# Optimization experiments

Measured on AMD Instinct MI355X. Metric: run time of the kernel, lower is better.

The kernel has to match this reference:

```python
import jax, jax.numpy as jnp
import numpy as np

B, L, D, H = 32, 1024, 1024, 1024

def setup_inputs() -> dict:
    key = jax.random.key(0)
    k1, k2, k3 = jax.random.split(key, 3)
    query = jax.random.normal(k1, (B, L, D), dtype=jnp.float32)
    keys = jax.random.normal(k2, (B, L, D), dtype=jnp.float32)
    # xavier_normal for Linear(D, H): std = sqrt(2/(D+H))
    W = jax.random.normal(k3, (H, D), dtype=jnp.float32) * np.sqrt(2.0 / (D + H)).astype(np.float32)
    b = jnp.zeros((H,), dtype=jnp.float32)
    return {"query": query, "keys": keys, "W": W, "b": b}

def reference(query, keys, W, b):
    # L2-normalize along feature dim (matches torch .norm(dim=-1, keepdim=True))
    qn = query / jnp.linalg.norm(query, axis=-1, keepdims=True)
    kn = keys / jnp.linalg.norm(keys, axis=-1, keepdims=True)
    # scores[b,i,j] = <kn[b,i], qn[b,j]>  ->  [B, Lk, Lq]
    scores = jnp.einsum('bid,bjd->bij', kn, qn)
    attn = jax.nn.softmax(scores, axis=-1)
    # bmm(attn, keys) then sum over batch -> [L, D]
    out = jnp.einsum('bij,bjd->id', attn, keys)
    x = jax.nn.relu(out @ W.T + b)
    return (x, attn)
```

## Files before the change

kernel.cpp:

```cpp
#include <hip/hip_runtime.h>
#include <hip/hip_bf16.h>

#define NBATCH 32
#define Ls 1024
#define Ds 1024
#define Hs 1024

typedef float f32x4 __attribute__((ext_vector_type(4)));
typedef __bf16 v8bf __attribute__((ext_vector_type(8)));
typedef unsigned short u16x8 __attribute__((ext_vector_type(8)));
typedef unsigned short u16x4 __attribute__((ext_vector_type(4)));
typedef __hip_bfloat16 bf16;

__device__ __forceinline__ float bfbits2f(unsigned short h) {
  unsigned u = ((unsigned)h) << 16;
  return __builtin_bit_cast(float, u);
}
__device__ __forceinline__ unsigned short f2b(float x) {
  return __builtin_bit_cast(unsigned short, __float2bfloat16(x));
}
__device__ __forceinline__ u16x8 pack8(const float4& a, const float4& b, float s) {
  u16x8 r;
  r[0] = f2b(a.x * s); r[1] = f2b(a.y * s); r[2] = f2b(a.z * s); r[3] = f2b(a.w * s);
  r[4] = f2b(b.x * s); r[5] = f2b(b.y * s); r[6] = f2b(b.z * s); r[7] = f2b(b.w * s);
  return r;
}

__global__ __launch_bounds__(256) void k_convq(const float* __restrict__ q,
                                               bf16* __restrict__ qn) {
  const int w0 = ((int)blockIdx.x * 256 + (int)threadIdx.x) >> 6;
  const int lane = threadIdx.x & 63;
  #pragma unroll
  for (int it = 0; it < 2; ++it) {
    const size_t r0 = ((size_t)(it * 8192 + w0)) * 2;
    const float4* q0 = reinterpret_cast<const float4*>(q + r0 * Ds);
    float4 qv[2][4];
    #pragma unroll
    for (int rr = 0; rr < 2; ++rr)
      #pragma unroll
      for (int h = 0; h < 2; ++h) {
        qv[rr][h * 2 + 0] = q0[rr * 256 + h * 128 + lane * 2 + 0];
        qv[rr][h * 2 + 1] = q0[rr * 256 + h * 128 + lane * 2 + 1];
      }
    float sq0 = 0.f, sq1 = 0.f;
    #pragma unroll
    for (int p = 0; p < 4; ++p) {
      sq0 += qv[0][p].x*qv[0][p].x + qv[0][p].y*qv[0][p].y + qv[0][p].z*qv[0][p].z + qv[0][p].w*qv[0][p].w;
      sq1 += qv[1][p].x*qv[1][p].x + qv[1][p].y*qv[1][p].y + qv[1][p].z*qv[1][p].z + qv[1][p].w*qv[1][p].w;
    }
    #pragma unroll
    for (int o = 1; o < 64; o <<= 1) { sq0 += __shfl_xor(sq0, o); sq1 += __shfl_xor(sq1, o); }
    const float iq0 = 1.0f / sqrtf(sq0), iq1 = 1.0f / sqrtf(sq1);
    u16x8* qo = reinterpret_cast<u16x8*>(qn + r0 * Ds);
    qo[lane]        = pack8(qv[0][0], qv[0][1], iq0);
    qo[64 + lane]   = pack8(qv[0][2], qv[0][3], iq0);
    qo[128 + lane]  = pack8(qv[1][0], qv[1][1], iq1);
    qo[192 + lane]  = pack8(qv[1][2], qv[1][3], iq1);
  }
}

__global__ __launch_bounds__(256) void k_convkT(const float* __restrict__ k,
                                                bf16* __restrict__ kb,
                                                bf16* __restrict__ kT,
                                                float* __restrict__ invk) {
  __shared__ float tile[64][65];
  __shared__ float red[4][16][16];
  const int b = blockIdx.y;
  const int j0 = blockIdx.x * 64;
  const int t = threadIdx.x;
  const int jr = t >> 4;
  const int cg = t & 15;
  const int c4 = cg * 4;
  const float* src = k + (size_t)b * Ls * Ds + (size_t)j0 * Ds;
  bf16* kbd = kb + (size_t)b * Ls * Ds + (size_t)j0 * Ds;
  bf16* kTd = kT + (size_t)b * Ds * Ls + j0;
  float ssq[4] = {0.f, 0.f, 0.f, 0.f};

  for (int dc = 0; dc < 16; ++dc) {
    const int d0 = dc * 64;
    float4 v[4];
    #pragma unroll
    for (int rr = 0; rr < 4; ++rr) {
      const int j = jr + rr * 16;
      v[rr] = *reinterpret_cast<const float4*>(&src[(size_t)j * Ds + d0 + c4]);
      ssq[rr] += v[rr].x*v[rr].x + v[rr].y*v[rr].y + v[rr].z*v[rr].z + v[rr].w*v[rr].w;
      u16x4 o = { f2b(v[rr].x), f2b(v[rr].y), f2b(v[rr].z), f2b(v[rr].w) };
      *reinterpret_cast<u16x4*>(&kbd[(size_t)j * Ds + d0 + c4]) = o;
    }
    __syncthreads();
    #pragma unroll
    for (int rr = 0; rr < 4; ++rr) {
      const int j = jr + rr * 16;
      tile[j][c4 + 0] = v[rr].x; tile[j][c4 + 1] = v[rr].y;
      tile[j][c4 + 2] = v[rr].z; tile[j][c4 + 3] = v[rr].w;
    }
    __syncthreads();
    #pragma unroll
    for (int rr = 0; rr < 4; ++rr) {
      const int dd = jr + rr * 16;
      u16x4 o = { f2b(tile[c4 + 0][dd]), f2b(tile[c4 + 1][dd]),
                  f2b(tile[c4 + 2][dd]), f2b(tile[c4 + 3][dd]) };
      *reinterpret_cast<u16x4*>(&kTd[(size_t)(d0 + dd) * Ls + c4]) = o;
    }
  }

  #pragma unroll
  for (int rr = 0; rr < 4; ++rr) red[rr][jr][cg] = ssq[rr];
  __syncthreads();
  if (t < 64) {
    const int r = (t & 15) + (t >> 4) * 16;
    float s = 0.f;
    #pragma unroll
    for (int c = 0; c < 16; ++c) s += red[t >> 4][t & 15][c];
    invk[(size_t)b * Ls + j0 + r] = 1.0f / sqrtf(s);
  }
}

__global__ __launch_bounds__(256) void k_w2(const float* __restrict__ W,
                                            bf16* __restrict__ W2) {
  const size_t idx = (size_t)blockIdx.x * 256 + threadIdx.x;
  const size_t e0 = idx * 4;
  const size_t h = e0 >> 10, d = e0 & 1023;
  const float4 w = reinterpret_cast<const float4*>(W)[idx];
  u16x4 wh = { f2b(w.x), f2b(w.y), f2b(w.z), f2b(w.w) };
  u16x4 wl = { f2b(w.x - bfbits2f(wh[0])), f2b(w.y - bfbits2f(wh[1])),
               f2b(w.z - bfbits2f(wh[2])), f2b(w.w - bfbits2f(wh[3])) };
  bf16* row = W2 + h * 3072;
  *reinterpret_cast<u16x4*>(row + d) = wh;
  *reinterpret_cast<u16x4*>(row + 1024 + d) = wh;
  *reinterpret_cast<u16x4*>(row + 2048 + d) = wl;
}

template<int KT, int MODE>
__global__ __launch_bounds__(512) void k_gemm256(
    const bf16* __restrict__ A, const bf16* __restrict__ B,
    void* __restrict__ Cv, const float* __restrict__ scale,
    int lda, int ldb, int ldc, int nb,
    size_t sA, size_t sB, size_t zA, size_t zB, size_t zC, size_t zS)
{
  __shared__ bf16 lds[2][2][256 * 64];
  const int tid = threadIdx.x;
  const int lane = tid & 63;
  const int wid = tid >> 6;
  const int wr = wid >> 2;
  const int wc = wid & 3;
  const int bid = blockIdx.x;
  const int bz = (bid & 7) + 8 * (bid >> 7);
  const int wq = (bid >> 3) & 15;
  const size_t n0 = (size_t)(wq & 3) * 256;
  const size_t m0 = (size_t)(wq >> 2) * 256;
  const bf16* Az = A + (size_t)bz * zA;
  const bf16* Bz = B + (size_t)bz * zB;

  const int srow = tid >> 3;
  const int sslot = tid & 7;
  f32x4 acc[8][4] = {};

  auto stageChunk = [&](int tt, int ab, int c, int buf) {
    const int bb = tt / KT;
    const int k0 = (tt - bb * KT) * 64;
    const int row = c * 64 + srow;
    const int ksl = (sslot ^ (row & 7)) * 8;
    const bf16* src = (ab == 0)
        ? (Az + (size_t)bb * sA + (m0 + row) * lda + k0 + ksl)
        : (Bz + (size_t)bb * sB + (n0 + row) * ldb + k0 + ksl);
    __builtin_amdgcn_global_load_lds(
        (const __attribute__((address_space(1))) void*)src,
        (__attribute__((address_space(3))) void*)(&lds[buf][ab][c * 4096 + tid * 8]), 16, 0, 0);
  };

  const int rsel = lane & 15, qd = lane >> 4;
  v8bf a0[4][2], a1[4][2], b[4][2];

  auto readAinto = [&](v8bf (&dst)[4][2], const bf16* As, int mh) {
    #pragma unroll
    for (int m = 0; m < 4; ++m) {
      const int r = wr * 128 + mh * 64 + m * 16 + rsel;
      #pragma unroll
      for (int h = 0; h < 2; ++h) {
        const int s = (h * 4 + qd) ^ (r & 7);
        dst[m][h] = *reinterpret_cast<const v8bf*>(reinterpret_cast<const char*>(As) + r * 128 + s * 16);
      }
    }
  };
  auto readB2 = [&](const bf16* Bs, int npair) {
    #pragma unroll
    for (int n = 0; n < 2; ++n) {
      const int r = wc * 64 + (npair * 2 + n) * 16 + rsel;
      #pragma unroll
      for (int h = 0; h < 2; ++h) {
        const int s = (h * 4 + qd) ^ (r & 7);
        b[npair * 2 + n][h] = *reinterpret_cast<const v8bf*>(reinterpret_cast<const char*>(Bs) + r * 128 + s * 16);
      }
    }
  };
  auto mfmaQ = [&](v8bf (&aa)[4][2], int mh, int npair) {
    __builtin_amdgcn_s_setprio(1);
    #pragma unroll
    for (int m = 0; m < 4; ++m)
      #pragma unroll
      for (int n = 0; n < 2; ++n) {
        const int mi = mh * 4 + m, ni = npair * 2 + n;
        acc[mi][ni] = __builtin_amdgcn_mfma_f32_16x16x32_bf16(aa[m][0], b[ni][0], acc[mi][ni], 0, 0, 0);
        acc[mi][ni] = __builtin_amdgcn_mfma_f32_16x16x32_bf16(aa[m][1], b[ni][1], acc[mi][ni], 0, 0, 0);
      }
    __builtin_amdgcn_s_setprio(0);
  };

  const int T = KT * nb;

  #pragma unroll
  for (int c = 0; c < 4; ++c) stageChunk(0, 0, c, 0);
  #pragma unroll
  for (int c = 0; c < 4; ++c) stageChunk(0, 1, c, 0);
  #pragma unroll
  for (int c = 0; c < 4; ++c) stageChunk(1, 0, c, 1);
  #pragma unroll
  for (int c = 0; c < 4; ++c) stageChunk(1, 1, c, 1);
  asm volatile("s_waitcnt vmcnt(8)" ::: "memory");
  __builtin_amdgcn_s_barrier();

  for (int t = 0; t < T; ++t) {
    const int d = t & 1;
    const bf16* As = lds[d][0];
    const bf16* Bs = lds[d][1];
    const int u = t + 2;
    const bool st = (u < T);

    readAinto(a0, As, 0);
    readB2(Bs, 0);
    __builtin_amdgcn_sched_barrier(0);
    readB2(Bs, 1);
    __builtin_amdgcn_sched_barrier(0);
    readAinto(a1, As, 1);
    __builtin_amdgcn_sched_barrier(0);

    asm volatile("s_waitcnt lgkmcnt(12)" ::: "memory");
    __builtin_amdgcn_sched_barrier(0);
    mfmaQ(a0, 0, 0);
    asm volatile("s_waitcnt lgkmcnt(8)" ::: "memory");
    __builtin_amdgcn_sched_barrier(0);
    mfmaQ(a0, 0, 1);
    asm volatile("s_waitcnt lgkmcnt(0)" ::: "memory");
    __builtin_amdgcn_sched_barrier(0);
    __builtin_amdgcn_s_barrier();
    if (st) {
      stageChunk(u, 0, 0, d); stageChunk(u, 0, 1, d);
      stageChunk(u, 0, 2, d); stageChunk(u, 0, 3, d);
      stageChunk(u, 1, 0, d); stageChunk(u, 1, 1, d);
      stageChunk(u, 1, 2, d); stageChunk(u, 1, 3, d);
    }
    __builtin_amdgcn_sched_barrier(0);
    mfmaQ(a1, 1, 1);
    mfmaQ(a1, 1, 0);
    if (t < T - 1) {
      if (st) { asm volatile("s_waitcnt vmcnt(8)" ::: "memory"); }
      else    { asm volatile("s_waitcnt vmcnt(0)" ::: "memory"); }
      __builtin_amdgcn_s_barrier();
    }
  }

  if (MODE == 0) {
    float* Cz = (float*)Cv + (size_t)bz * zC;
    #pragma unroll
    for (int m = 0; m < 8; ++m) {
      const size_t ri = m0 + wr * 128 + m * 16 + (size_t)((lane >> 4) * 4);
      #pragma unroll
      for (int n = 0; n < 4; ++n) {
        const size_t cj = n0 + wc * 64 + n * 16 + (lane & 15);
        #pragma unroll
        for (int r = 0; r < 4; ++r)
          Cz[(ri + r) * ldc + cj] = acc[m][n][r];
      }
    }
  } else {
    bf16* Cz = (bf16*)Cv + (size_t)bz * zC;
    const float* Sz = scale + (size_t)bz * zS;
    #pragma unroll
    for (int m = 0; m < 8; ++m) {
      const size_t ri = m0 + wr * 128 + m * 16 + (size_t)((lane >> 4) * 4);
      const float4 ik = *reinterpret_cast<const float4*>(Sz + ri);
      #pragma unroll
      for (int n = 0; n < 4; ++n) {
        const size_t cj = n0 + wc * 64 + n * 16 + (lane & 15);
        Cz[(ri + 0) * ldc + cj] = __float2bfloat16(acc[m][n][0] * ik.x);
        Cz[(ri + 1) * ldc + cj] = __float2bfloat16(acc[m][n][1] * ik.y);
        Cz[(ri + 2) * ldc + cj] = __float2bfloat16(acc[m][n][2] * ik.z);
        Cz[(ri + 3) * ldc + cj] = __float2bfloat16(acc[m][n][3] * ik.w);
      }
    }
  }
}

__global__ __launch_bounds__(256) void k_gemm_nt(
    const bf16* __restrict__ A, const bf16* __restrict__ B,
    float* __restrict__ C,
    int lda, int ldb, int ldc, int K,
    size_t zA, size_t zB, size_t zC)
{
  __shared__ bf16 As[128 * 32];
  __shared__ bf16 Bs[128 * 32];
  const int tid = threadIdx.x;
  const int lane = tid & 63;
  const int wc = (tid >> 6) & 1;
  const int wr = (tid >> 7) & 1;
  const size_t m0 = (size_t)blockIdx.y * 128;
  const size_t n0 = (size_t)blockIdx.x * 128;
  const bf16* Az = A + (size_t)blockIdx.z * zA;
  const bf16* Bz = B + (size_t)blockIdx.z * zB;
  float* Cz = C + (size_t)blockIdx.z * zC;
  f32x4 acc[4][4] = {};

  const int beta0 = tid * 16;
  const int row0 = tid >> 2;
  const int kk0 = ((tid & 3) ^ ((row0 >> 1) & 3)) * 8;
  const int sw = (((lane >> 4) ^ ((lane >> 1) & 3)) << 4);
  const int rsel = lane & 15;

  for (int k0 = 0; k0 < K; k0 += 32) {
    __syncthreads();
    __builtin_amdgcn_global_load_lds(
        (const __attribute__((address_space(1))) void*)(Az + (m0 + row0) * lda + (k0 + kk0)),
        (__attribute__((address_space(3))) void*)(&As[beta0 / 2]), 16, 0, 0);
    __builtin_amdgcn_global_load_lds(
        (const __attribute__((address_space(1))) void*)(Az + (m0 + row0 + 64) * lda + (k0 + kk0)),
        (__attribute__((address_space(3))) void*)(&As[beta0 / 2 + 2048]), 16, 0, 0);
    __builtin_amdgcn_global_load_lds(
        (const __attribute__((address_space(1))) void*)(Bz + (n0 + row0) * ldb + (k0 + kk0)),
        (__attribute__((address_space(3))) void*)(&Bs[beta0 / 2]), 16, 0, 0);
    __builtin_amdgcn_global_load_lds(
        (const __attribute__((address_space(1))) void*)(Bz + (n0 + row0 + 64) * ldb + (k0 + kk0)),
        (__attribute__((address_space(3))) void*)(&Bs[beta0 / 2 + 2048]), 16, 0, 0);
    __syncthreads();

    v8bf af[4], bg[4];
    #pragma unroll
    for (int m = 0; m < 4; ++m) {
      const int rA = wr * 64 + m * 16 + rsel;
      af[m] = *reinterpret_cast<const v8bf*>(reinterpret_cast<const char*>(As) + rA * 64 + sw);
      const int rB = wc * 64 + m * 16 + rsel;
      bg[m] = *reinterpret_cast<const v8bf*>(reinterpret_cast<const char*>(Bs) + rB * 64 + sw);
    }
    #pragma unroll
    for (int m = 0; m < 4; ++m)
      #pragma unroll
      for (int n = 0; n < 4; ++n)
        acc[m][n] = __builtin_amdgcn_mfma_f32_16x16x32_bf16(af[m], bg[n], acc[m][n], 0, 0, 0);
  }

  #pragma unroll
  for (int m = 0; m < 4; ++m) {
    const size_t ri = m0 + wr * 64 + m * 16 + ((lane >> 4) * 4);
    #pragma unroll
    for (int n = 0; n < 4; ++n) {
      const size_t cj = n0 + wc * 64 + n * 16 + (lane & 15);
      #pragma unroll
      for (int r = 0; r < 4; ++r)
        Cz[(ri + r) * ldc + cj] = acc[m][n][r];
    }
  }
}

__global__ __launch_bounds__(256) void k_softmax(const bf16* __restrict__ sc,
                                                 float* __restrict__ attn,
                                                 bf16* __restrict__ abf) {
  const int wave = ((int)blockIdx.x * 256 + (int)threadIdx.x) >> 6;
  const int lane = threadIdx.x & 63;
  for (int i = 0; i < 4; ++i) {
    const size_t row = (size_t)wave * 4 + i;
    const u16x8* sr = reinterpret_cast<const u16x8*>(sc + row * Ls);
    const u16x8 s0 = sr[lane], s1 = sr[lane + 64];
    float e[16];
    float ss = 0.f;
    #pragma unroll
    for (int j = 0; j < 8; ++j) { e[j] = __expf(bfbits2f(s0[j])); ss += e[j]; }
    #pragma unroll
    for (int j = 0; j < 8; ++j) { e[8 + j] = __expf(bfbits2f(s1[j])); ss += e[8 + j]; }
    #pragma unroll
    for (int o = 1; o < 64; o <<= 1) ss += __shfl_xor(ss, o);
    const float inv = 1.0f / ss;
    #pragma unroll
    for (int j = 0; j < 16; ++j) e[j] *= inv;
    float4* ar = reinterpret_cast<float4*>(attn + row * Ls);
    float4 a0 = {e[0], e[1], e[2], e[3]},   a1 = {e[4], e[5], e[6], e[7]};
    float4 a2 = {e[8], e[9], e[10], e[11]}, a3 = {e[12], e[13], e[14], e[15]};
    ar[lane * 2 + 0] = a0;  ar[lane * 2 + 1] = a1;
    ar[128 + lane * 2 + 0] = a2;  ar[128 + lane * 2 + 1] = a3;
    u16x8* ab8 = reinterpret_cast<u16x8*>(abf + row * Ls);
    u16x8 b0, b1;
    #pragma unroll
    for (int j = 0; j < 8; ++j) { b0[j] = f2b(e[j]); b1[j] = f2b(e[8 + j]); }
    ab8[lane] = b0;
    ab8[64 + lane] = b1;
  }
}

__global__ __launch_bounds__(256) void k_reduce(const float* __restrict__ part,
                                                bf16* __restrict__ A2) {
  const size_t idx = (size_t)blockIdx.x * 256 + threadIdx.x;
  float4 s = {0.f, 0.f, 0.f, 0.f};
  #pragma unroll
  for (int g = 0; g < 16; ++g) {
    const float4 p = reinterpret_cast<const float4*>(part + (size_t)g * (Ls * Ds))[idx];
    s.x += p.x; s.y += p.y; s.z += p.z; s.w += p.w;
  }
  const size_t e0 = idx * 4;
  const size_t i = e0 >> 10, d = e0 & 1023;
  u16x4 h = { f2b(s.x), f2b(s.y), f2b(s.z), f2b(s.w) };
  u16x4 l = { f2b(s.x - bfbits2f(h[0])), f2b(s.y - bfbits2f(h[1])),
              f2b(s.z - bfbits2f(h[2])), f2b(s.w - bfbits2f(h[3])) };
  bf16* row = A2 + i * 3072;
  *reinterpret_cast<u16x4*>(row + d) = h;
  *reinterpret_cast<u16x4*>(row + 1024 + d) = l;
  *reinterpret_cast<u16x4*>(row + 2048 + d) = h;
}

__global__ __launch_bounds__(256) void k_reduce2(const float* __restrict__ part2,
                                                 const float* __restrict__ bias,
                                                 float* __restrict__ xout) {
  const size_t idx = (size_t)blockIdx.x * 256 + threadIdx.x;
  float4 s = {0.f, 0.f, 0.f, 0.f};
  #pragma unroll
  for (int g = 0; g < 4; ++g) {
    const float4 p = reinterpret_cast<const float4*>(part2 + (size_t)g * (Ls * Hs))[idx];
    s.x += p.x; s.y += p.y; s.z += p.z; s.w += p.w;
  }
  const size_t h0 = (idx * 4) & 1023;
  const float4 bv = *reinterpret_cast<const float4*>(bias + h0);
  s.x = fmaxf(s.x + bv.x, 0.f); s.y = fmaxf(s.y + bv.y, 0.f);
  s.z = fmaxf(s.z + bv.z, 0.f); s.w = fmaxf(s.w + bv.w, 0.f);
  reinterpret_cast<float4*>(xout)[idx] = s;
}

extern "C" void kernel_launch(void* const* d_in, const int* in_sizes, int n_in,
                              void* d_out, int out_size, void* d_ws, size_t ws_size,
                              hipStream_t stream) {
  const float* q = (const float*)d_in[0];
  const float* k = (const float*)d_in[1];
  const float* W = (const float*)d_in[2];
  const float* bias = (const float*)d_in[3];
  float* xout = (float*)d_out;
  float* attn = (float*)d_out + (size_t)Ls * Hs;

  char* w = (char*)d_ws;
  bf16* qn    = (bf16*)w;
  bf16* kb    = (bf16*)(w + ((size_t)64 << 20));
  bf16* kT    = (bf16*)(w + ((size_t)128 << 20));
  bf16* sc_bf = (bf16*)(w + ((size_t)192 << 20));
  bf16* W2    = (bf16*)(w + ((size_t)256 << 20));
  bf16* A2    = (bf16*)(w + ((size_t)263 << 20));
  float* invk = (float*)(w + ((size_t)270 << 20));
  float* part  = (float*)kb;
  float* part2 = (float*)kT;
  bf16* abf = qn;

  k_convq<<<2048, 256, 0, stream>>>(q, qn);
  k_convkT<<<dim3(16, NBATCH), 256, 0, stream>>>(k, kb, kT, invk);
  k_w2<<<(Hs * Ds / 4) / 256, 256, 0, stream>>>(W, W2);

  k_gemm256<16, 1><<<512, 512, 0, stream>>>(kb, qn, sc_bf, invk,
      Ds, Ds, Ls, 1,
      (size_t)Ls * Ds, (size_t)Ls * Ds,
      (size_t)Ls * Ds, (size_t)Ls * Ds, (size_t)Ls * Ls, (size_t)Ls);

  k_softmax<<<2048, 256, 0, stream>>>(sc_bf, attn, abf);

  k_gemm256<16, 0><<<256, 512, 0, stream>>>(abf, kT, part, nullptr,
      Ls, Ls, Ds, 2,
      (size_t)Ls * Ls, (size_t)Ls * Ds,
      (size_t)2 * Ls * Ls, (size_t)2 * Ls * Ds, (size_t)Ls * Ds, 0);

  k_reduce<<<(Ls * Ds / 4) / 256, 256, 0, stream>>>(part, A2);

  k_gemm_nt<<<dim3(8, 8, 4), 256, 0, stream>>>(A2, W2, part2,
      3072, 3072, Hs, 768, 768, 768, (size_t)Ls * Hs);

  k_reduce2<<<(Ls * Hs / 4) / 256, 256, 0, stream>>>(part2, bias, xout);
}
```

Measured before the change: 343.0 us.

## Replace double-buffered LDS pipeline with single-buffer synchronous staging in GEMM

```diff
diff --git a/kernel.cpp b/kernel.cpp
--- a/kernel.cpp
+++ b/kernel.cpp
@@ -138,7 +138,7 @@
     int lda, int ldb, int ldc, int nb,
     size_t sA, size_t sB, size_t zA, size_t zB, size_t zC, size_t zS)
 {
-  __shared__ bf16 lds[2][2][256 * 64];
+  __shared__ bf16 lds[2][256 * 64];
   const int tid = threadIdx.x;
   const int lane = tid & 63;
   const int wid = tid >> 6;
@@ -156,7 +156,7 @@
   const int sslot = tid & 7;
   f32x4 acc[8][4] = {};
 
-  auto stageChunk = [&](int tt, int ab, int c, int buf) {
+  auto stageChunk = [&](int tt, int ab, int c) {
     const int bb = tt / KT;
     const int k0 = (tt - bb * KT) * 64;
     const int row = c * 64 + srow;
@@ -166,13 +166,14 @@
         : (Bz + (size_t)bb * sB + (n0 + row) * ldb + k0 + ksl);
     __builtin_amdgcn_global_load_lds(
         (const __attribute__((address_space(1))) void*)src,
-        (__attribute__((address_space(3))) void*)(&lds[buf][ab][c * 4096 + tid * 8]), 16, 0, 0);
+        (__attribute__((address_space(3))) void*)(&lds[ab][c * 4096 + tid * 8]), 16, 0, 0);
   };
 
   const int rsel = lane & 15, qd = lane >> 4;
   v8bf a0[4][2], a1[4][2], b[4][2];
 
-  auto readAinto = [&](v8bf (&dst)[4][2], const bf16* As, int mh) {
+  auto readAinto = [&](v8bf (&dst)[4][2], int mh) {
+    const bf16* As = lds[0];
     #pragma unroll
     for (int m = 0; m < 4; ++m) {
       const int r = wr * 128 + mh * 64 + m * 16 + rsel;
@@ -183,7 +184,8 @@
       }
     }
   };
-  auto readB2 = [&](const bf16* Bs, int npair) {
+  auto readB2 = [&](int npair) {
+    const bf16* Bs = lds[1];
     #pragma unroll
     for (int n = 0; n < 2; ++n) {
       const int r = wc * 64 + (npair * 2 + n) * 16 + rsel;
@@ -209,55 +211,20 @@
 
   const int T = KT * nb;
 
-  #pragma unroll
-  for (int c = 0; c < 4; ++c) stageChunk(0, 0, c, 0);
-  #pragma unroll
-  for (int c = 0; c < 4; ++c) stageChunk(0, 1, c, 0);
-  #pragma unroll
-  for (int c = 0; c < 4; ++c) stageChunk(1, 0, c, 1);
-  #pragma unroll
-  for (int c = 0; c < 4; ++c) stageChunk(1, 1, c, 1);
-  asm volatile("s_waitcnt vmcnt(8)" ::: "memory");
-  __builtin_amdgcn_s_barrier();
-
   for (int t = 0; t < T; ++t) {
-    const int d = t & 1;
-    const bf16* As = lds[d][0];
-    const bf16* Bs = lds[d][1];
-    const int u = t + 2;
-    const bool st = (u < T);
-
-    readAinto(a0, As, 0);
-    readB2(Bs, 0);
-    __builtin_amdgcn_sched_barrier(0);
-    readB2(Bs, 1);
-    __builtin_amdgcn_sched_barrier(0);
-    readAinto(a1, As, 1);
-    __builtin_amdgcn_sched_barrier(0);
-
-    asm volatile("s_waitcnt lgkmcnt(12)" ::: "memory");
-    __builtin_amdgcn_sched_barrier(0);
+    __syncthreads();
+    #pragma unroll
+    for (int c = 0; c < 4; ++c) stageChunk(t, 0, c);
+    #pragma unroll
+    for (int c = 0; c < 4; ++c) stageChunk(t, 1, c);
+    __syncthreads();
+
+    readAinto(a0, 0); readB2(0); readB2(1);
     mfmaQ(a0, 0, 0);
-    asm volatile("s_waitcnt lgkmcnt(8)" ::: "memory");
-    __builtin_amdgcn_sched_barrier(0);
     mfmaQ(a0, 0, 1);
-    asm volatile("s_waitcnt lgkmcnt(0)" ::: "memory");
-    __builtin_amdgcn_sched_barrier(0);
-    __builtin_amdgcn_s_barrier();
-    if (st) {
-      stageChunk(u, 0, 0, d); stageChunk(u, 0, 1, d);
-      stageChunk(u, 0, 2, d); stageChunk(u, 0, 3, d);
-      stageChunk(u, 1, 0, d); stageChunk(u, 1, 1, d);
-      stageChunk(u, 1, 2, d); stageChunk(u, 1, 3, d);
-    }
-    __builtin_amdgcn_sched_barrier(0);
+    readAinto(a1, 1);
     mfmaQ(a1, 1, 1);
     mfmaQ(a1, 1, 0);
-    if (t < T - 1) {
-      if (st) { asm volatile("s_waitcnt vmcnt(8)" ::: "memory"); }
-      else    { asm volatile("s_waitcnt vmcnt(0)" ::: "memory"); }
-      __builtin_amdgcn_s_barrier();
-    }
   }
 
   if (MODE == 0) {
```

Result: slower. 399.1 us (+16.4%).
